# Optimization experiments

Hardware: AMD Instinct MI355X
Metric: run time of the kernel (lower is better)

The kernel has to match this reference:

```python
import jax, jax.numpy as jnp
import numpy as np

NUM_VERTS = 6890
NUM_FACES = 13776
MAX_COLLISIONS = 8      # BVH(max_collisions=8)
SIGMA = 0.5             # df_cone_height
POINT2PLANE = False
PENALIZE_OUTSIDE = True
COLL_LOSS_WEIGHT = 1.0
EPS = 1e-8


def setup_inputs() -> dict:
    key = jax.random.key(0)
    k1, k2 = jax.random.split(key)
    vertices = jax.random.normal(k1, (1, NUM_VERTS, 3), dtype=jnp.float32)
    # flat face index list, as consumed by index_select(vertices, 1, faces)
    faces = jax.random.randint(k2, (NUM_FACES * 3,), 0, NUM_VERTS, dtype=jnp.int32)
    return {"vertices": vertices, "faces": faces}


def _find_collisions(triangles, faces_mat):
    """Fixed-shape emulation of the BVH broad phase.

    triangles: [B,F,3,3]. Returns collision_idxs [B, F*K, 2] int32 with -1 padding,
    pairs (receiver, intruder) whose AABBs overlap, excluding pairs of triangles
    that share a vertex (as the BVH does; this also removes self-pairs).
    """
    B, F = triangles.shape[0], triangles.shape[1]
    bbmin = triangles.min(axis=2)   # [B,F,3]
    bbmax = triangles.max(axis=2)   # [B,F,3]
    overlap = jnp.ones((B, F, F), dtype=bool)
    for a in range(3):  # fixed 3-axis loop
        lo = bbmin[:, :, a]
        hi = bbmax[:, :, a]
        overlap = overlap & (lo[:, :, None] <= hi[:, None, :]) & (lo[:, None, :] <= hi[:, :, None])
    # triangles sharing any vertex are never reported as collisions
    share = jnp.zeros((F, F), dtype=bool)
    for a in range(3):
        for b in range(3):
            share = share | (faces_mat[:, a][:, None] == faces_mat[:, b][None, :])
    valid = overlap & ~share[None]
    vals, idxs = jax.lax.top_k(valid.astype(jnp.float32), MAX_COLLISIONS)  # [B,F,K]
    intr = jnp.where(vals > 0, idxs, -1)
    recv = jnp.broadcast_to(jnp.arange(F, dtype=jnp.int32)[None, :, None], intr.shape)
    recv = jnp.where(intr >= 0, recv, -1)
    return jnp.stack([recv.reshape(B, -1), intr.reshape(B, -1)], axis=-1)  # [B,F*K,2]


def _cone_field_penalty(src_tri, pts):
    """Conical distance-field penalty (Tzionas et al.) of src triangles
    evaluated at the 3 vertices of the paired triangle.
    src_tri: [B,P,3,3] field-generating triangles; pts: [B,P,3,3] query vertices.
    Returns per-pair penalty [B,P].
    """
    e0 = src_tri[..., 1, :] - src_tri[..., 0, :]
    e1 = src_tri[..., 2, :] - src_tri[..., 0, :]
    n = jnp.cross(e0, e1)
    n = n / (jnp.linalg.norm(n, axis=-1, keepdims=True) + EPS)  # unit normal
    c = src_tri.mean(axis=-2)                                    # triangle center
    u = pts - c[..., None, :]                                    # [B,P,3,3]
    h = jnp.sum(u * n[..., None, :], axis=-1)                    # signed height [B,P,3]
    r = jnp.linalg.norm(u - h[..., None] * n[..., None, :], axis=-1)  # radial dist
    radial = jax.nn.relu(1.0 - r / SIGMA)        # linear falloff of the cone
    depth = jax.nn.relu(-h)                      # penetration depth behind the face
    if PENALIZE_OUTSIDE:
        depth = depth + jax.nn.relu(h) * jnp.exp(-h / SIGMA)  # soft outside penalty
    phi = radial * depth
    per_v = radial * h * h if POINT2PLANE else phi * phi
    return per_v.sum(axis=-1)  # sum over the 3 query vertices -> [B,P]


def reference(vertices, faces):
    B = vertices.shape[0]
    triangles = vertices[:, faces, :].reshape(B, -1, 3, 3)  # [B,F,3,3]
    faces_mat = faces.reshape(-1, 3)
    # collision search runs under no_grad in the original
    coll = _find_collisions(jax.lax.stop_gradient(triangles), faces_mat)  # [B,P,2]
    valid = (coll[..., 0] >= 0)
    recv_idx = jnp.maximum(coll[..., 0], 0)
    intr_idx = jnp.maximum(coll[..., 1], 0)
    bi = jnp.arange(B)[:, None]
    recv_tri = triangles[bi, recv_idx]  # [B,P,3,3]
    intr_tri = triangles[bi, intr_idx]  # [B,P,3,3]
    pen = _cone_field_penalty(recv_tri, intr_tri) + _cone_field_penalty(intr_tri, recv_tri)
    return COLL_LOSS_WEIGHT * jnp.sum(jnp.where(valid, pen, 0.0))
```

## Files before the change

### kernel.cpp

```cpp
#include <hip/hip_runtime.h>

#define NF   13776
#define NFP  13824
#define KMAX 8
#define EPS  1e-8f
#define CBLK 2048

__global__ __launch_bounds__(256) void prep_kernel(
    const float* __restrict__ verts,
    const int*   __restrict__ faces,
    float4* __restrict__ tri,
    float4* __restrict__ lo4, float4* __restrict__ hi4,
    int* __restrict__ f2)
{
    int f = blockIdx.x * blockDim.x + threadIdx.x;
    if (f >= NFP) return;
    if (f >= NF) {
        lo4[f] = make_float4(INFINITY, INFINITY, INFINITY, __int_as_float(-1));
        hi4[f] = make_float4(-INFINITY, -INFINITY, -INFINITY, __int_as_float(-1));
        f2[f]  = -1;
        return;
    }
    int ia = faces[3 * f + 0], ib = faces[3 * f + 1], ic = faces[3 * f + 2];
    float ax = verts[3 * ia + 0], ay = verts[3 * ia + 1], az = verts[3 * ia + 2];
    float bx = verts[3 * ib + 0], by = verts[3 * ib + 1], bz = verts[3 * ib + 2];
    float cx = verts[3 * ic + 0], cy = verts[3 * ic + 1], cz = verts[3 * ic + 2];
    tri[3 * f + 0] = make_float4(ax, ay, az, bx);
    tri[3 * f + 1] = make_float4(by, bz, cx, cy);
    tri[3 * f + 2] = make_float4(cz, 0.f, 0.f, 0.f);
    lo4[f] = make_float4(fminf(ax, fminf(bx, cx)),
                         fminf(ay, fminf(by, cy)),
                         fminf(az, fminf(bz, cz)), __int_as_float(ia));
    hi4[f] = make_float4(fmaxf(ax, fmaxf(bx, cx)),
                         fmaxf(ay, fmaxf(by, cy)),
                         fmaxf(az, fmaxf(bz, cz)), __int_as_float(ib));
    f2[f] = ic;
}

__device__ __forceinline__ float cone_pen_v(const float* s,
                                            float px, float py, float pz) {
    float e0x = s[3] - s[0], e0y = s[4] - s[1], e0z = s[5] - s[2];
    float e1x = s[6] - s[0], e1y = s[7] - s[1], e1z = s[8] - s[2];
    float nx = e0y * e1z - e0z * e1y;
    float ny = e0z * e1x - e0x * e1z;
    float nz = e0x * e1y - e0y * e1x;
    float inv = 1.0f / (sqrtf(nx * nx + ny * ny + nz * nz) + EPS);
    nx *= inv; ny *= inv; nz *= inv;
    const float third = 1.0f / 3.0f;
    float cx = (s[0] + s[3] + s[6]) * third;
    float cy = (s[1] + s[4] + s[7]) * third;
    float cz = (s[2] + s[5] + s[8]) * third;
    float ux = px - cx, uy = py - cy, uz = pz - cz;
    float h = ux * nx + uy * ny + uz * nz;
    float rx = ux - h * nx, ry = uy - h * ny, rz = uz - h * nz;
    float r = sqrtf(rx * rx + ry * ry + rz * rz);
    float radial = fmaxf(0.0f, 1.0f - 2.0f * r);
    float depth = (h < 0.0f) ? -h : h * expf(-2.0f * h);
    float phi = radial * depth;
    return phi * phi;
}

__global__ __launch_bounds__(256) void coll_kernel(
    const float4* __restrict__ tri,
    const float4* __restrict__ lo4, const float4* __restrict__ hi4,
    const int* __restrict__ f2,
    float* __restrict__ partial)
{
    const int lane = threadIdx.x & 63;
    const int wid  = threadIdx.x >> 6;
    const int gw   = (blockIdx.x * blockDim.x + threadIdx.x) >> 6;
    const int nw   = (gridDim.x * blockDim.x) >> 6;

    float acc = 0.0f;

    for (int i = gw; i < NF; i += nw) {
        float4 rlo = lo4[i], rhi = hi4[i];
        int fa0 = __float_as_int(rlo.w);
        int fa1 = __float_as_int(rhi.w);
        int fa2 = f2[i];

        int nc = 0;
        int hj = -1;
        for (int base = 0; base < NFP && nc < KMAX; base += 64) {
            int j = base + lane;
            float4 jlo = lo4[j];
            float4 jhi = hi4[j];
            int jf2 = f2[j];
            bool ov = (rlo.x <= jhi.x) & (jlo.x <= rhi.x)
                    & (rlo.y <= jhi.y) & (jlo.y <= rhi.y)
                    & (rlo.z <= jhi.z) & (jlo.z <= rhi.z);
            int fb0 = __float_as_int(jlo.w);
            int fb1 = __float_as_int(jhi.w);
            bool share = (fb0 == fa0) | (fb0 == fa1) | (fb0 == fa2)
                       | (fb1 == fa0) | (fb1 == fa1) | (fb1 == fa2)
                       | (jf2 == fa0) | (jf2 == fa1) | (jf2 == fa2);
            bool valid = ov & !share;
            unsigned long long mask = __ballot(valid);
            int cnt  = __popcll(mask);
            int take = min(cnt, KMAX - nc);
            if (lane >= nc && lane < nc + take) {
                int t = lane - nc;
                unsigned long long m = mask;
                for (int q = 0; q < t; ++q) m &= (m - 1);
                hj = base + __builtin_ctzll(m);
            }
            nc += take;
        }

        int k = lane >> 3;
        int t = lane & 7;
        int hjk = __shfl(hj, k);
        float p = 0.0f;
        if (t < 6 && k < nc) {
            int d = (t >= 3) ? 1 : 0;
            int v = t - 3 * d;
            int si = d ? hjk : i;
            int qi = d ? i : hjk;
            float4 s0 = tri[3 * si + 0];
            float4 s1 = tri[3 * si + 1];
            float4 s2 = tri[3 * si + 2];
            float s[9] = { s0.x, s0.y, s0.z, s0.w, s1.x, s1.y, s1.z, s1.w, s2.x };
            const float* qp = (const float*)(tri + 3 * qi);
            p = cone_pen_v(s, qp[3 * v + 0], qp[3 * v + 1], qp[3 * v + 2]);
        }
        acc += p;
    }

#pragma unroll
    for (int off = 32; off > 0; off >>= 1) acc += __shfl_xor(acc, off);
    __shared__ float wsum[4];
    if (lane == 0) wsum[wid] = acc;
    __syncthreads();
    if (threadIdx.x == 0)
        partial[blockIdx.x] = wsum[0] + wsum[1] + wsum[2] + wsum[3];
}

__global__ __launch_bounds__(256) void reduce_kernel(
    const float* __restrict__ partial, float* __restrict__ out)
{
    float a = 0.0f;
    for (int idx = threadIdx.x; idx < CBLK; idx += 256) a += partial[idx];
#pragma unroll
    for (int off = 32; off > 0; off >>= 1) a += __shfl_xor(a, off);
    __shared__ float ws[4];
    int lane = threadIdx.x & 63, wid = threadIdx.x >> 6;
    if (lane == 0) ws[wid] = a;
    __syncthreads();
    if (threadIdx.x == 0) out[0] = ws[0] + ws[1] + ws[2] + ws[3];
}

extern "C" void kernel_launch(void* const* d_in, const int* in_sizes, int n_in,
                              void* d_out, int out_size, void* d_ws, size_t ws_size,
                              hipStream_t stream) {
    const float* verts = (const float*)d_in[0];
    const int*   faces = (const int*)d_in[1];
    float* out = (float*)d_out;

    float4* tri = (float4*)d_ws;
    float4* lo4 = tri + NFP * 3;
    float4* hi4 = lo4 + NFP;
    int*    f2  = (int*)(hi4 + NFP);
    float*  partial = (float*)(f2 + NFP);

    prep_kernel<<<NFP / 256, 256, 0, stream>>>(verts, faces, tri, lo4, hi4, f2);
    coll_kernel<<<CBLK, 256, 0, stream>>>(tri, lo4, hi4, f2, partial);
    reduce_kernel<<<1, 256, 0, stream>>>(partial, out);
}
```

Measured before the change: 66.74 us.

## Pack third face index into AABB pad and process two receivers per wave

Packs the first and third vertex indices of each face into the w lane of the lower AABB as 16-bit halves, so the separate f2 array and its per-candidate load go away. Each wave now handles exactly two receiver faces, i and i+6888. The first 64-candidate chunk is shared between them, then each gets its own early-exit scan, and the grid shrinks to 1722 blocks with no grid-stride loop. The penalty stage evaluates both receivers unconditionally and masks the dead lanes. This relies on vertex indices fitting in 16 bits (6890 verts) and on the padding sentinel -1 not matching any packed field.

```diff
diff --git a/kernel.cpp b/kernel.cpp
--- a/kernel.cpp
+++ b/kernel.cpp
@@ -2,23 +2,22 @@
 
 #define NF   13776
 #define NFP  13824
+#define HALF 6888
 #define KMAX 8
 #define EPS  1e-8f
-#define CBLK 2048
+#define CBLK 1722
 
 __global__ __launch_bounds__(256) void prep_kernel(
     const float* __restrict__ verts,
     const int*   __restrict__ faces,
     float4* __restrict__ tri,
-    float4* __restrict__ lo4, float4* __restrict__ hi4,
-    int* __restrict__ f2)
+    float4* __restrict__ lo4, float4* __restrict__ hi4)
 {
     int f = blockIdx.x * blockDim.x + threadIdx.x;
     if (f >= NFP) return;
     if (f >= NF) {
         lo4[f] = make_float4(INFINITY, INFINITY, INFINITY, __int_as_float(-1));
         hi4[f] = make_float4(-INFINITY, -INFINITY, -INFINITY, __int_as_float(-1));
-        f2[f]  = -1;
         return;
     }
     int ia = faces[3 * f + 0], ib = faces[3 * f + 1], ic = faces[3 * f + 2];
@@ -30,11 +29,12 @@
     tri[3 * f + 2] = make_float4(cz, 0.f, 0.f, 0.f);
     lo4[f] = make_float4(fminf(ax, fminf(bx, cx)),
                          fminf(ay, fminf(by, cy)),
-                         fminf(az, fminf(bz, cz)), __int_as_float(ia));
+                         fminf(az, fminf(bz, cz)),
+                         __int_as_float((ia & 0xFFFF) | (ic << 16)));
     hi4[f] = make_float4(fmaxf(ax, fmaxf(bx, cx)),
                          fmaxf(ay, fmaxf(by, cy)),
-                         fmaxf(az, fmaxf(bz, cz)), __int_as_float(ib));
-    f2[f] = ic;
+                         fmaxf(az, fmaxf(bz, cz)),
+                         __int_as_float(ib));
 }
 
 __device__ __forceinline__ float cone_pen_v(const float* s,
@@ -60,71 +60,109 @@
     return phi * phi;
 }
 
+__device__ __forceinline__ bool valid_pair(
+    const float4& rlo, const float4& rhi, int fa0, int fa1, int fa2,
+    const float4& jlo, const float4& jhi)
+{
+    bool ov = (rlo.x <= jhi.x) & (jlo.x <= rhi.x)
+            & (rlo.y <= jhi.y) & (jlo.y <= rhi.y)
+            & (rlo.z <= jhi.z) & (jlo.z <= rhi.z);
+    int w0  = __float_as_int(jlo.w);
+    int fb0 = w0 & 0xFFFF;
+    int fb2 = ((unsigned)w0) >> 16;
+    int fb1 = __float_as_int(jhi.w);
+    bool share = (fb0 == fa0) | (fb0 == fa1) | (fb0 == fa2)
+               | (fb1 == fa0) | (fb1 == fa1) | (fb1 == fa2)
+               | (fb2 == fa0) | (fb2 == fa1) | (fb2 == fa2);
+    return ov & !share;
+}
+
+__device__ __forceinline__ void take_hits(bool valid, int base, int lane,
+                                          int& nc, int& hj)
+{
+    unsigned long long mask = __ballot(valid);
+    int cnt  = __popcll(mask);
+    int take = min(cnt, KMAX - nc);
+    if (lane >= nc && lane < nc + take) {
+        int t = lane - nc;
+        unsigned long long m = mask;
+        for (int q = 0; q < t; ++q) m &= (m - 1);
+        hj = base + __builtin_ctzll(m);
+    }
+    nc += take;
+}
+
+__device__ __forceinline__ float pen_term(const float4* __restrict__ tri,
+                                          int i, int hjk, int d, int v,
+                                          bool live)
+{
+    int jj = max(hjk, 0);
+    int si = d ? jj : i;
+    int qi = d ? i : jj;
+    float4 s0 = tri[3 * si + 0];
+    float4 s1 = tri[3 * si + 1];
+    float4 s2 = tri[3 * si + 2];
+    float4 q0 = tri[3 * qi + 0];
+    float4 q1 = tri[3 * qi + 1];
+    float4 q2 = tri[3 * qi + 2];
+    float px = (v == 0) ? q0.x : ((v == 1) ? q0.w : q1.z);
+    float py = (v == 0) ? q0.y : ((v == 1) ? q1.x : q1.w);
+    float pz = (v == 0) ? q0.z : ((v == 1) ? q1.y : q2.x);
+    float s[9] = { s0.x, s0.y, s0.z, s0.w, s1.x, s1.y, s1.z, s1.w, s2.x };
+    float p = cone_pen_v(s, px, py, pz);
+    return live ? p : 0.0f;
+}
+
 __global__ __launch_bounds__(256) void coll_kernel(
     const float4* __restrict__ tri,
     const float4* __restrict__ lo4, const float4* __restrict__ hi4,
-    const int* __restrict__ f2,
     float* __restrict__ partial)
 {
     const int lane = threadIdx.x & 63;
     const int wid  = threadIdx.x >> 6;
     const int gw   = (blockIdx.x * blockDim.x + threadIdx.x) >> 6;
-    const int nw   = (gridDim.x * blockDim.x) >> 6;
-
-    float acc = 0.0f;
-
-    for (int i = gw; i < NF; i += nw) {
-        float4 rlo = lo4[i], rhi = hi4[i];
-        int fa0 = __float_as_int(rlo.w);
-        int fa1 = __float_as_int(rhi.w);
-        int fa2 = f2[i];
-
-        int nc = 0;
-        int hj = -1;
-        for (int base = 0; base < NFP && nc < KMAX; base += 64) {
-            int j = base + lane;
-            float4 jlo = lo4[j];
-            float4 jhi = hi4[j];
-            int jf2 = f2[j];
-            bool ov = (rlo.x <= jhi.x) & (jlo.x <= rhi.x)
-                    & (rlo.y <= jhi.y) & (jlo.y <= rhi.y)
-                    & (rlo.z <= jhi.z) & (jlo.z <= rhi.z);
-            int fb0 = __float_as_int(jlo.w);
-            int fb1 = __float_as_int(jhi.w);
-            bool share = (fb0 == fa0) | (fb0 == fa1) | (fb0 == fa2)
-                       | (fb1 == fa0) | (fb1 == fa1) | (fb1 == fa2)
-                       | (jf2 == fa0) | (jf2 == fa1) | (jf2 == fa2);
-            bool valid = ov & !share;
-            unsigned long long mask = __ballot(valid);
-            int cnt  = __popcll(mask);
-            int take = min(cnt, KMAX - nc);
-            if (lane >= nc && lane < nc + take) {
-                int t = lane - nc;
-                unsigned long long m = mask;
-                for (int q = 0; q < t; ++q) m &= (m - 1);
-                hj = base + __builtin_ctzll(m);
-            }
-            nc += take;
-        }
-
-        int k = lane >> 3;
-        int t = lane & 7;
-        int hjk = __shfl(hj, k);
-        float p = 0.0f;
-        if (t < 6 && k < nc) {
-            int d = (t >= 3) ? 1 : 0;
-            int v = t - 3 * d;
-            int si = d ? hjk : i;
-            int qi = d ? i : hjk;
-            float4 s0 = tri[3 * si + 0];
-            float4 s1 = tri[3 * si + 1];
-            float4 s2 = tri[3 * si + 2];
-            float s[9] = { s0.x, s0.y, s0.z, s0.w, s1.x, s1.y, s1.z, s1.w, s2.x };
-            const float* qp = (const float*)(tri + 3 * qi);
-            p = cone_pen_v(s, qp[3 * v + 0], qp[3 * v + 1], qp[3 * v + 2]);
-        }
-        acc += p;
-    }
+
+    const int iA = gw;
+    const int iB = gw + HALF;
+
+    float4 rloA = lo4[iA], rhiA = hi4[iA];
+    float4 rloB = lo4[iB], rhiB = hi4[iB];
+    int wA0 = __float_as_int(rloA.w);
+    int faA0 = wA0 & 0xFFFF, faA2 = ((unsigned)wA0) >> 16;
+    int faA1 = __float_as_int(rhiA.w);
+    int wB0 = __float_as_int(rloB.w);
+    int faB0 = wB0 & 0xFFFF, faB2 = ((unsigned)wB0) >> 16;
+    int faB1 = __float_as_int(rhiB.w);
+
+    int ncA = 0, ncB = 0, hjA = -1, hjB = -1;
+
+    {
+        float4 jlo = lo4[lane], jhi = hi4[lane];
+        bool vA = valid_pair(rloA, rhiA, faA0, faA1, faA2, jlo, jhi);
+        bool vB = valid_pair(rloB, rhiB, faB0, faB1, faB2, jlo, jhi);
+        take_hits(vA, 0, lane, ncA, hjA);
+        take_hits(vB, 0, lane, ncB, hjB);
+    }
+    for (int base = 64; base < NFP && ncA < KMAX; base += 64) {
+        float4 jlo = lo4[base + lane], jhi = hi4[base + lane];
+        bool vA = valid_pair(rloA, rhiA, faA0, faA1, faA2, jlo, jhi);
+        take_hits(vA, base, lane, ncA, hjA);
+    }
+    for (int base = 64; base < NFP && ncB < KMAX; base += 64) {
+        float4 jlo = lo4[base + lane], jhi = hi4[base + lane];
+        bool vB = valid_pair(rloB, rhiB, faB0, faB1, faB2, jlo, jhi);
+        take_hits(vB, base, lane, ncB, hjB);
+    }
+
+    int k = lane >> 3;
+    int t = lane & 7;
+    int d = (t >= 3) ? 1 : 0;
+    int v = t - 3 * d;
+    int hjkA = __shfl(hjA, k);
+    int hjkB = __shfl(hjB, k);
+    bool liveT = (t < 6);
+    float acc = pen_term(tri, iA, hjkA, d, v, liveT & (k < ncA))
+              + pen_term(tri, iB, hjkB, d, v, liveT & (k < ncB));
 
 #pragma unroll
     for (int off = 32; off > 0; off >>= 1) acc += __shfl_xor(acc, off);
@@ -159,10 +197,9 @@
     float4* tri = (float4*)d_ws;
     float4* lo4 = tri + NFP * 3;
     float4* hi4 = lo4 + NFP;
-    int*    f2  = (int*)(hi4 + NFP);
-    float*  partial = (float*)(f2 + NFP);
-
-    prep_kernel<<<NFP / 256, 256, 0, stream>>>(verts, faces, tri, lo4, hi4, f2);
-    coll_kernel<<<CBLK, 256, 0, stream>>>(tri, lo4, hi4, f2, partial);
+    float*  partial = (float*)(hi4 + NFP);
+
+    prep_kernel<<<NFP / 256, 256, 0, stream>>>(verts, faces, tri, lo4, hi4);
+    coll_kernel<<<CBLK, 256, 0, stream>>>(tri, lo4, hi4, partial);
     reduce_kernel<<<1, 256, 0, stream>>>(partial, out);
 }
```

New measurement: 67.63 us. No clear change (+1.3%).
